# Kernel tuning notes

Hardware: AMD Instinct MI355X
Metric: run time of the kernel (lower is better)

The kernel has to match this reference:

```python
import jax, jax.numpy as jnp
import numpy as np
from jax import lax

CONF_T = 0.5
IOU_T = 0.5
STRIDE = 8.0
NA = 3            # anchors per cell
NO = 16           # x,y,w,h,obj,10 landmarks,cls
G = 80            # grid size for 640/8
K = 300           # max detections kept into NMS
ANCHORS = np.array([[4., 5.], [8., 10.], [13., 16.]], dtype=np.float32)


def _conv(x, w, b, stride):
    y = lax.conv_general_dilated(x, w, (stride, stride), 'SAME',
                                 dimension_numbers=('NCHW', 'OIHW', 'NCHW'))
    return jax.nn.silu(y + b[None, :, None, None])


def _nms_single(boxes, scores):
    # boxes [N,4] xyxy, scores [N] (0 where below conf threshold)
    top_scores, idx = lax.top_k(scores, K)
    b = boxes[idx]                                   # [K,4]
    x1, y1, x2, y2 = b[:, 0], b[:, 1], b[:, 2], b[:, 3]
    area = jnp.maximum(x2 - x1, 0.) * jnp.maximum(y2 - y1, 0.)
    ix1 = jnp.maximum(x1[:, None], x1[None, :])
    iy1 = jnp.maximum(y1[:, None], y1[None, :])
    ix2 = jnp.minimum(x2[:, None], x2[None, :])
    iy2 = jnp.minimum(y2[:, None], y2[None, :])
    inter = jnp.maximum(ix2 - ix1, 0.) * jnp.maximum(iy2 - iy1, 0.)
    iou = inter / (area[:, None] + area[None, :] - inter + 1e-7)   # [K,K]

    ar = jnp.arange(K)

    def body(i, keep):
        sup = keep[i] & (iou[i] > IOU_T) & (ar > i)
        return keep & ~sup

    keep = lax.fori_loop(0, K, body, jnp.ones((K,), bool))
    keep = keep & (top_scores > 0.)
    return jnp.concatenate(
        [b, top_scores[:, None], keep.astype(b.dtype)[:, None]], axis=-1)  # [K,6]


def setup_inputs() -> dict:
    key = jax.random.key(0)
    ks = jax.random.split(key, 9)
    s = 0.1
    return {
        'x':  jax.random.uniform(ks[0], (16, 3, 640, 640), jnp.float32),
        'W1': jax.random.normal(ks[1], (16, 3, 3, 3), jnp.float32) * s,
        'b1': jnp.zeros((16,), jnp.float32),
        'W2': jax.random.normal(ks[2], (32, 16, 3, 3), jnp.float32) * s,
        'b2': jnp.zeros((32,), jnp.float32),
        'W3': jax.random.normal(ks[3], (64, 32, 3, 3), jnp.float32) * s,
        'b3': jnp.zeros((64,), jnp.float32),
        'Wh': jax.random.normal(ks[4], (NA * NO, 64, 1, 1), jnp.float32) * s,
        'bh': jnp.zeros((NA * NO,), jnp.float32),
    }


def reference(x, W1, b1, W2, b2, W3, b3, Wh, bh):
    B = x.shape[0]
    # backbone: stride-8 conv stem (YOLOv5n-like)
    f = _conv(x, W1, b1, 2)      # [B,16,320,320]
    f = _conv(f, W2, b2, 2)      # [B,32,160,160]
    f = _conv(f, W3, b3, 2)      # [B,64,80,80]
    h = lax.conv_general_dilated(f, Wh, (1, 1), 'SAME',
                                 dimension_numbers=('NCHW', 'OIHW', 'NCHW'))
    h = h + bh[None, :, None, None]                  # [B,NA*NO,G,G]
    p = h.reshape(B, NA, NO, G, G).transpose(0, 1, 3, 4, 2)  # [B,NA,G,G,NO]
    p = jax.nn.sigmoid(p)

    gy, gx = jnp.meshgrid(jnp.arange(G, dtype=jnp.float32),
                          jnp.arange(G, dtype=jnp.float32), indexing='ij')
    grid = jnp.stack([gx, gy], axis=-1)              # [G,G,2]
    anchors = jnp.asarray(ANCHORS)

    xy = (p[..., 0:2] * 2. - 0.5 + grid[None, None]) * STRIDE
    wh = (p[..., 2:4] * 2.) ** 2 * anchors[None, :, None, None, :]
    score = p[..., 4] * p[..., 15]                   # obj * cls

    boxes = jnp.concatenate([xy - wh / 2., xy + wh / 2.], axis=-1)
    boxes = boxes.reshape(B, -1, 4)                  # [B,N,4]
    score = score.reshape(B, -1)                     # [B,N]
    score = jnp.where(score > CONF_T, score, 0.)

    return jax.vmap(_nms_single)(boxes, score)       # [B,K,6]
```

## Files before the change

### kernel.cpp

```cpp
#include <hip/hip_runtime.h>
#include <math.h>

#define BATCH 16
#define GRID  80
#define NANCH 3
#define KTOP  300
#define NBOX  (NANCH*GRID*GRID)
#define SORT_CAP 8192

__device__ __forceinline__ float sigmoidf_(float x){ return 1.0f/(1.0f+expf(-x)); }

template<int CIN,int COUT,int C,int ICCH,int HIN,int HOUT,int TX,int TY>
__global__ __launch_bounds__(256, 1) void conv3x3s2_v7(
    const float* __restrict__ in, const float* __restrict__ w,
    const float* __restrict__ bias, float* __restrict__ out)
{
  constexpr int NTX = TX/4, NTY = TY/2, NSP = NTX*NTY, OCG = COUT/C;
  static_assert(NSP*OCG == 256, "bad thread layout");
  static_assert(C==4 || C==8, "C must be 4 or 8");
  constexpr int HR = 2*TY+1, HC = 2*TX+1;
  constexpr int NB4  = HC/4;
  constexpr int PADC = ((HC+3)/4)*4 + 4;
  constexpr int ILDSC = HR*PADC;
  constexpr int TBX = HOUT/TX, TBY = HOUT/TY;
  static_assert(TBX*TX == HOUT && TBY*TY == HOUT, "no masking");
  constexpr int NCH  = CIN/ICCH;
  constexpr int NH4  = ICCH*HR*NB4;
  constexpr int NH1  = ICCH*HR;
  constexpr int NWT  = ICCH*9*COUT;
  constexpr int NLD4 = (NH4+255)/256;
  constexpr int NLD1 = (NH1+255)/256;
  constexpr int NLDW = (NWT+255)/256;
  __shared__ float ilds[2][ICCH*ILDSC];
  __shared__ float wlds[2][NWT];

  const int t  = threadIdx.x;
  const int sx = t % NTX;
  const int sy = (t / NTX) % NTY;
  const int og = t / NSP;
  int blk = blockIdx.x;
  const int bx = blk % TBX; blk /= TBX;
  const int by = blk % TBY; blk /= TBY;
  const int b  = blk;

  const int ix0 = bx*2*TX, iy0 = by*2*TY;
  const int ylim = (iy0 + HR <= HIN) ? HR : (HIN - iy0);
  const bool tail_ok = (ix0 + NB4*4 < HIN);

  float4 hreg[NLD4];
  float  treg[NLD1];
  float  wreg[NLDW];

  auto load_regs = [&](int c0){
    #pragma unroll
    for (int l=0;l<NLD4;++l){
      int i = t + 256*l;
      float4 v = make_float4(0.f,0.f,0.f,0.f);
      if (i < NH4){
        int c = i/(HR*NB4), rm = i - c*(HR*NB4);
        int r = rm/NB4, m = rm - r*NB4;
        if (r < ylim)
          v = *(const float4*)(in + (size_t)(b*CIN + c0 + c)*HIN*HIN
                                  + (size_t)(iy0+r)*HIN + ix0 + 4*m);
      }
      hreg[l] = v;
    }
    #pragma unroll
    for (int l=0;l<NLD1;++l){
      int i = t + 256*l;
      float v = 0.f;
      if (i < NH1){
        int c = i/HR, r = i - c*HR;
        if (r < ylim && tail_ok)
          v = in[(size_t)(b*CIN + c0 + c)*HIN*HIN + (size_t)(iy0+r)*HIN + ix0 + NB4*4];
      }
      treg[l] = v;
    }
    #pragma unroll
    for (int l=0;l<NLDW;++l){
      int i = t + 256*l;
      float v = 0.f;
      if (i < NWT){
        int oc  = i % COUT;
        int k   = (i / COUT) % 9;
        int icl = i / (9*COUT);
        v = w[((size_t)oc*CIN + c0+icl)*9 + k];
      }
      wreg[l] = v;
    }
  };

  auto write_lds = [&](int bufi){
    #pragma unroll
    for (int l=0;l<NLD4;++l){
      int i = t + 256*l;
      if (i < NH4){
        int c = i/(HR*NB4), rm = i - c*(HR*NB4);
        int r = rm/NB4, m = rm - r*NB4;
        *(float4*)(&ilds[bufi][c*ILDSC + r*PADC + 4*((r>>2)&1) + 4*m]) = hreg[l];
      }
    }
    #pragma unroll
    for (int l=0;l<NLD1;++l){
      int i = t + 256*l;
      if (i < NH1){
        int c = i/HR, r = i - c*HR;
        ilds[bufi][c*ILDSC + r*PADC + 4*((r>>2)&1) + NB4*4] = treg[l];
      }
    }
    #pragma unroll
    for (int l=0;l<NLDW;++l){
      int i = t + 256*l;
      if (i < NWT) wlds[bufi][i] = wreg[l];
    }
  };

  float acc[C][2][4];
  #pragma unroll
  for (int j=0;j<C;++j){
    float bv = bias[og*C+j];
    #pragma unroll
    for (int py=0;py<2;++py)
      #pragma unroll
      for (int px=0;px<4;++px) acc[j][py][px]=bv;
  }

  load_regs(0);
  write_lds(0);
  __syncthreads();

  #pragma unroll 1
  for (int ch=0; ch<NCH; ++ch){
    const int cur = ch & 1;
    if (ch+1 < NCH) load_regs((ch+1)*ICCH);

    #pragma unroll 1
    for (int icl=0; icl<ICCH; ++icl){
      const float* wpb = &wlds[cur][icl*9*COUT] + og*C;
      float4 wk0[9], wk1[9];
      #pragma unroll
      for (int k=0;k<9;++k){
        wk0[k] = *(const float4*)(wpb + k*COUT);
        if constexpr (C==8) wk1[k] = *(const float4*)(wpb + k*COUT + 4);
      }
      const float* ipb = &ilds[cur][icl*ILDSC] + 8*sx;
      float rw[5][12];
      #pragma unroll
      for (int r=0;r<5;++r){
        const int rr = 4*sy + r;
        const float* rp = ipb + rr*PADC + 4*((rr>>2)&1);
        #pragma unroll
        for (int m=0;m<3;++m){
          float4 v4 = *(const float4*)(rp + 4*m);
          rw[r][4*m+0]=v4.x; rw[r][4*m+1]=v4.y; rw[r][4*m+2]=v4.z; rw[r][4*m+3]=v4.w;
        }
      }
      #pragma unroll
      for (int py=0;py<2;++py)
        #pragma unroll
        for (int ky=0;ky<3;++ky)
          #pragma unroll
          for (int kx=0;kx<3;++kx){
            const float4 wa = wk0[ky*3+kx];
            #pragma unroll
            for (int px=0;px<4;++px){
              const float xv = rw[2*py+ky][2*px+kx];
              acc[0][py][px] += xv*wa.x; acc[1][py][px] += xv*wa.y;
              acc[2][py][px] += xv*wa.z; acc[3][py][px] += xv*wa.w;
            }
            if constexpr (C==8){
              const float4 wb = wk1[ky*3+kx];
              #pragma unroll
              for (int px=0;px<4;++px){
                const float xv = rw[2*py+ky][2*px+kx];
                acc[4][py][px] += xv*wb.x; acc[5][py][px] += xv*wb.y;
                acc[6][py][px] += xv*wb.z; acc[7][py][px] += xv*wb.w;
              }
            }
          }
    }

    if (ch+1 < NCH) write_lds((ch+1)&1);
    __syncthreads();
  }

  const int oxb = bx*TX + sx*4;
  #pragma unroll
  for (int j=0;j<C;++j){
    int oc = og*C+j;
    #pragma unroll
    for (int py=0;py<2;++py){
      int oy = by*TY + sy*2 + py;
      float4 o4;
      float z0=acc[j][py][0], z1=acc[j][py][1], z2=acc[j][py][2], z3=acc[j][py][3];
      o4.x = z0/(1.0f+expf(-z0));
      o4.y = z1/(1.0f+expf(-z1));
      o4.z = z2/(1.0f+expf(-z2));
      o4.w = z3/(1.0f+expf(-z3));
      *(float4*)(out + ((size_t)(b*COUT+oc)*HOUT + oy)*HOUT + oxb) = o4;
    }
  }
}

__global__ __launch_bounds__(256) void decode_kernel(
    const float* __restrict__ f3, const float* __restrict__ Wh,
    const float* __restrict__ bh, float* __restrict__ boxes,
    float* __restrict__ scores)
{
  int idx = blockIdx.x*256 + threadIdx.x;
  const int total = BATCH*NANCH*GRID*GRID;
  if (idx >= total) return;
  int gx = idx % GRID;
  int gy = (idx/GRID)%GRID;
  int a  = (idx/(GRID*GRID))%NANCH;
  int b  = idx/(GRID*GRID*NANCH);
  const float aw[3] = {4.0f, 8.0f, 13.0f};
  const float ah[3] = {5.0f, 10.0f, 16.0f};
  const int   chs[6] = {0,1,2,3,4,15};
  const float* f = f3 + (size_t)b*64*GRID*GRID + (size_t)gy*GRID + gx;
  float acc[6];
  #pragma unroll
  for (int j=0;j<6;j++) acc[j] = bh[a*16 + chs[j]];
  for (int ic=0; ic<64; ++ic){
    float v = f[(size_t)ic*GRID*GRID];
    #pragma unroll
    for (int j=0;j<6;j++) acc[j] += v * Wh[(size_t)(a*16+chs[j])*64 + ic];
  }
  float p0 = sigmoidf_(acc[0]);
  float p1 = sigmoidf_(acc[1]);
  float p2 = sigmoidf_(acc[2]);
  float p3 = sigmoidf_(acc[3]);
  float p4 = sigmoidf_(acc[4]);
  float p15= sigmoidf_(acc[5]);
  float cx = (p0*2.0f - 0.5f + (float)gx)*8.0f;
  float cy = (p1*2.0f - 0.5f + (float)gy)*8.0f;
  float ww = p2*2.0f; ww = ww*ww*aw[a];
  float hh = p3*2.0f; hh = hh*hh*ah[a];
  float sc = p4*p15;
  sc = (sc > 0.5f) ? sc : 0.0f;
  int bi = a*GRID*GRID + gy*GRID + gx;
  float* bo = boxes + ((size_t)b*NBOX + bi)*4;
  bo[0] = cx - ww*0.5f;
  bo[1] = cy - hh*0.5f;
  bo[2] = cx + ww*0.5f;
  bo[3] = cy + hh*0.5f;
  scores[(size_t)b*NBOX + bi] = sc;
}

__global__ __launch_bounds__(1024) void topk_kernel(
    const float* __restrict__ boxes, const float* __restrict__ scores,
    float* __restrict__ nmsbuf, int* __restrict__ mcnt)
{
  __shared__ unsigned long long keys[SORT_CAP];
  __shared__ int   cntM;
  __shared__ int   sel[KTOP];
  __shared__ float selsc[KTOP];
  __shared__ int   wsum[16];
  __shared__ float rs[16];
  __shared__ int   ri[16];
  __shared__ unsigned clm[(NBOX+31)/32];

  const int b = blockIdx.x;
  const int t = threadIdx.x;
  const int lane = t & 63, wv = t >> 6;
  const float* scp = scores + (size_t)b*NBOX;

  if (t == 0) cntM = 0;
  __syncthreads();

  for (int i=t; i<NBOX; i+=1024){
    float v = scp[i];
    if (v > 0.0f){
      int p = atomicAdd(&cntM, 1);
      if (p < SORT_CAP)
        keys[p] = ((unsigned long long)__float_as_uint(v) << 32)
                | (unsigned)(0xFFFFFFFFu - (unsigned)i);
    }
  }
  __syncthreads();
  const int M = cntM;
  if (t == 0) mcnt[b] = M;

  if (M <= SORT_CAP){
    int P = 64; while (P < M) P <<= 1;
    for (int i=t; i<P; i+=1024) if (i >= M) keys[i] = 0ULL;
    __syncthreads();
    for (int k=2; k<=P; k<<=1){
      for (int j=k>>1; j>0; j>>=1){
        for (int i=t; i<P; i+=1024){
          int ixj = i ^ j;
          if (ixj > i){
            unsigned long long a = keys[i], c = keys[ixj];
            bool up = ((i & k) == 0);
            if (up ? (a < c) : (a > c)){ keys[i] = c; keys[ixj] = a; }
          }
        }
        __syncthreads();
      }
    }
    const int top = (M < KTOP) ? M : KTOP;
    if (t < top){
      unsigned long long kk = keys[t];
      selsc[t] = __uint_as_float((unsigned)(kk >> 32));
      sel[t]   = (int)(0xFFFFFFFFu - (unsigned)(kk & 0xFFFFFFFFu));
    }
    if (M < KTOP){
      const int need = KTOP - M;
      const int C = (NBOX + 1023)/1024;
      int lo = t*C, hi = lo+C; if (hi > NBOX) hi = NBOX; if (lo > NBOX) lo = NBOX;
      int zc = 0;
      for (int i=lo;i<hi;i++) if (scp[i] <= 0.0f) zc++;
      int v = zc;
      #pragma unroll
      for (int off=1; off<64; off<<=1){
        int n = __shfl_up(v, off);
        if (lane >= off) v += n;
      }
      if (lane == 63) wsum[wv] = v;
      __syncthreads();
      if (t == 0){
        int a = 0;
        for (int w=0; w<16; w++){ int tmp = wsum[w]; wsum[w] = a; a += tmp; }
      }
      __syncthreads();
      int r = wsum[wv] + v - zc;
      for (int i=lo;i<hi;i++){
        if (scp[i] <= 0.0f){
          if (r < need){ sel[M+r] = i; selsc[M+r] = 0.0f; }
          r++;
        }
      }
    }
    __syncthreads();
  } else {
    for (int i=t; i<(NBOX+31)/32; i+=1024) clm[i] = 0u;
    __syncthreads();
    for (int k=0;k<KTOP;k++){
      float best = -2.0f; int bi = NBOX;
      for (int i=t;i<NBOX;i+=1024){
        if (!((clm[i>>5] >> (i&31)) & 1u)){
          float v = scp[i];
          if (v > best){ best=v; bi=i; }
        }
      }
      #pragma unroll
      for (int off=32; off>0; off>>=1){
        float ov = __shfl_down(best, off);
        int   oi = __shfl_down(bi,   off);
        if (ov > best || (ov == best && oi < bi)){ best=ov; bi=oi; }
      }
      if (lane == 0){ rs[wv]=best; ri[wv]=bi; }
      __syncthreads();
      if (t == 0){
        for (int w=1; w<16; w++)
          if (rs[w] > best || (rs[w] == best && ri[w] < bi)){ best=rs[w]; bi=ri[w]; }
        sel[k]=bi; selsc[k]=best; clm[bi>>5] |= (1u << (bi&31));
      }
      __syncthreads();
    }
  }

  if (t < KTOP){
    const float* bp = boxes + ((size_t)b*NBOX + sel[t])*4;
    float x1=bp[0], y1=bp[1], x2=bp[2], y2=bp[3];
    float* o = nmsbuf + ((size_t)b*KTOP + t)*6;
    o[0]=x1; o[1]=y1; o[2]=x2; o[3]=y2;
    o[4]=selsc[t];
    o[5]=fmaxf(x2-x1,0.0f)*fmaxf(y2-y1,0.0f);
  }
}

__global__ __launch_bounds__(64, 1) void nms_kernel(
    const float* __restrict__ nmsbuf, const int* __restrict__ mcnt,
    float* __restrict__ out)
{
  const int b = blockIdx.x;
  const int lane = threadIdx.x;
  int Mtop = mcnt[b]; if (Mtop > KTOP) Mtop = KTOP;
  float X1[5],Y1[5],X2[5],Y2[5],AR[5],SC[5];
  unsigned keepm = 0;
  #pragma unroll
  for (int s5=0; s5<5; ++s5){
    int j = lane + 64*s5;
    if (j < KTOP){
      const float* p = nmsbuf + ((size_t)b*KTOP + j)*6;
      X1[s5]=p[0]; Y1[s5]=p[1]; X2[s5]=p[2]; Y2[s5]=p[3];
      SC[s5]=p[4]; AR[s5]=p[5];
      keepm |= (1u << s5);
    } else { X1[s5]=0;Y1[s5]=0;X2[s5]=0;Y2[s5]=0;AR[s5]=0;SC[s5]=0; }
  }
  for (int i=0;i<Mtop;i++){
    const int iw = i & 63, is = i >> 6;
    unsigned km = __shfl(keepm, iw);
    if ((km >> is) & 1u){
      float sx1 = (is==0)?X1[0]:(is==1)?X1[1]:(is==2)?X1[2]:(is==3)?X1[3]:X1[4];
      float sy1 = (is==0)?Y1[0]:(is==1)?Y1[1]:(is==2)?Y1[2]:(is==3)?Y1[3]:Y1[4];
      float sx2 = (is==0)?X2[0]:(is==1)?X2[1]:(is==2)?X2[2]:(is==3)?X2[3]:X2[4];
      float sy2 = (is==0)?Y2[0]:(is==1)?Y2[1]:(is==2)?Y2[2]:(is==3)?Y2[3]:Y2[4];
      float sa  = (is==0)?AR[0]:(is==1)?AR[1]:(is==2)?AR[2]:(is==3)?AR[3]:AR[4];
      float bx1=__shfl(sx1,iw), by1=__shfl(sy1,iw);
      float bx2=__shfl(sx2,iw), by2=__shfl(sy2,iw);
      float ba =__shfl(sa ,iw);
      #pragma unroll
      for (int s5=0; s5<5; ++s5){
        int j = lane + 64*s5;
        if (((keepm >> s5) & 1u) && j > i){
          float ix1=fmaxf(bx1,X1[s5]);
          float iy1=fmaxf(by1,Y1[s5]);
          float ix2=fminf(bx2,X2[s5]);
          float iy2=fminf(by2,Y2[s5]);
          float inter=fmaxf(ix2-ix1,0.0f)*fmaxf(iy2-iy1,0.0f);
          float iou = inter/(ba+AR[s5]-inter+1e-7f);
          if (iou > 0.5f) keepm &= ~(1u << s5);
        }
      }
    }
  }
  #pragma unroll
  for (int s5=0; s5<5; ++s5){
    int j = lane + 64*s5;
    if (j < KTOP){
      float scv = SC[s5];
      float kf  = (((keepm >> s5) & 1u) && scv > 0.0f) ? 1.0f : 0.0f;
      float* o = out + ((size_t)b*KTOP + j)*6;
      o[0]=X1[s5]; o[1]=Y1[s5]; o[2]=X2[s5]; o[3]=Y2[s5];
      o[4]=scv; o[5]=kf;
    }
  }
}

extern "C" void kernel_launch(void* const* d_in, const int* in_sizes, int n_in,
                              void* d_out, int out_size, void* d_ws, size_t ws_size,
                              hipStream_t stream) {
  const float* x  = (const float*)d_in[0];
  const float* W1 = (const float*)d_in[1];
  const float* b1 = (const float*)d_in[2];
  const float* W2 = (const float*)d_in[3];
  const float* b2 = (const float*)d_in[4];
  const float* W3 = (const float*)d_in[5];
  const float* b3 = (const float*)d_in[6];
  const float* Wh = (const float*)d_in[7];
  const float* bh = (const float*)d_in[8];
  float* out = (float*)d_out;
  float* ws  = (float*)d_ws;

  float* f1     = ws;
  float* f2     = ws + 26214400;
  float* f3     = ws;
  float* boxes  = ws + 26214400;
  float* scores = boxes + 1228800;
  float* nmsbuf = scores + 307200;
  int*   mcnt   = (int*)(nmsbuf + 28800);

  conv3x3s2_v7<3,16,8,1,640,320,64,16><<<5*20*BATCH, 256, 0, stream>>>(x,  W1, b1, f1);
  conv3x3s2_v7<16,32,8,2,320,160,32,16><<<5*10*BATCH, 256, 0, stream>>>(f1, W2, b2, f2);
  conv3x3s2_v7<32,64,4,4,160,80,16,8><<<5*10*BATCH, 256, 0, stream>>>(f2, W3, b3, f3);

  decode_kernel<<<(BATCH*NANCH*GRID*GRID+255)/256, 256, 0, stream>>>(f3, Wh, bh, boxes, scores);
  topk_kernel<<<BATCH, 1024, 0, stream>>>(boxes, scores, nmsbuf, mcnt);
  nms_kernel<<<BATCH, 64, 0, stream>>>(nmsbuf, mcnt, out);
}
```

Before: 403.7 us.

## Fuse third conv with head decode and raise occupancy hint for conv2

Adds a kernel that computes the third 3x3 stride-2 conv and, inside the same block, stages the activated tile in shared memory to run the 1x1 head and box decode for the six needed channels. This removes the f3 write/read round trip and one kernel launch. Separately, conv2's launch bounds now request 4 waves per EU instead of 1, trading register budget for occupancy. The fused kernel reuses shared memory between the conv and decode phases, which adds an extra barrier and some per-block head-weight loads.

Measured after the change: 386.9 us. -4.2%, faster.

```diff
diff --git a/kernel.cpp b/kernel.cpp
--- a/kernel.cpp
+++ b/kernel.cpp
@@ -10,8 +10,8 @@
 
 __device__ __forceinline__ float sigmoidf_(float x){ return 1.0f/(1.0f+expf(-x)); }
 
-template<int CIN,int COUT,int C,int ICCH,int HIN,int HOUT,int TX,int TY>
-__global__ __launch_bounds__(256, 1) void conv3x3s2_v7(
+template<int CIN,int COUT,int C,int ICCH,int HIN,int HOUT,int TX,int TY,int MINW>
+__global__ __launch_bounds__(256, MINW) void conv3x3s2_v7(
     const float* __restrict__ in, const float* __restrict__ w,
     const float* __restrict__ bias, float* __restrict__ out)
 {
@@ -202,49 +202,235 @@
   }
 }
 
-__global__ __launch_bounds__(256) void decode_kernel(
-    const float* __restrict__ f3, const float* __restrict__ Wh,
-    const float* __restrict__ bh, float* __restrict__ boxes,
-    float* __restrict__ scores)
+__global__ __launch_bounds__(256, 1) void conv3_decode_fused(
+    const float* __restrict__ in,
+    const float* __restrict__ w,
+    const float* __restrict__ bias,
+    const float* __restrict__ wh,
+    const float* __restrict__ bh,
+    float* __restrict__ boxes, float* __restrict__ scores)
 {
-  int idx = blockIdx.x*256 + threadIdx.x;
-  const int total = BATCH*NANCH*GRID*GRID;
-  if (idx >= total) return;
-  int gx = idx % GRID;
-  int gy = (idx/GRID)%GRID;
-  int a  = (idx/(GRID*GRID))%NANCH;
-  int b  = idx/(GRID*GRID*NANCH);
-  const float aw[3] = {4.0f, 8.0f, 13.0f};
-  const float ah[3] = {5.0f, 10.0f, 16.0f};
-  const int   chs[6] = {0,1,2,3,4,15};
-  const float* f = f3 + (size_t)b*64*GRID*GRID + (size_t)gy*GRID + gx;
-  float acc[6];
+  constexpr int CIN=32, COUT=64, C=4, ICCH=4, HIN=160, TX=16, TY=8;
+  constexpr int NTX=TX/4, NTY=TY/2, NSP=NTX*NTY;
+  constexpr int HR=2*TY+1, HC=2*TX+1;
+  constexpr int NB4=HC/4;
+  constexpr int PADC=((HC+3)/4)*4+4;
+  constexpr int ILDSC=HR*PADC;
+  constexpr int TBX=5, TBY=10;
+  constexpr int NCH=CIN/ICCH;
+  constexpr int NH4=ICCH*HR*NB4;
+  constexpr int NH1=ICCH*HR;
+  constexpr int NWT=ICCH*9*COUT;
+  constexpr int NLD4=(NH4+255)/256, NLD1=(NH1+255)/256, NLDW=(NWT+255)/256;
+  __shared__ float smem[11232];
+  float* ildsb = smem;
+  float* wldsb = smem + 5440;
+  float* f3l   = smem;
+  float* whl   = smem + 10048;
+  float* bhl   = smem + 11200;
+
+  const int t  = threadIdx.x;
+  const int sx = t % NTX;
+  const int sy = (t / NTX) % NTY;
+  const int og = t / NSP;
+  int blk = blockIdx.x;
+  const int bx = blk % TBX; blk /= TBX;
+  const int by = blk % TBY; blk /= TBY;
+  const int b  = blk;
+
+  {
+    const int chs[6] = {0,1,2,3,4,15};
+    for (int i=t; i<1152; i+=256){
+      int row = i >> 6, ic = i & 63;
+      int a = row/6, j = row - 6*a;
+      whl[i] = wh[(size_t)(a*16+chs[j])*64 + ic];
+    }
+    if (t < 18){ int a=t/6, j=t-6*a; bhl[t] = bh[a*16+chs[j]]; }
+  }
+
+  const int ix0 = bx*2*TX, iy0 = by*2*TY;
+  const int ylim = (iy0 + HR <= HIN) ? HR : (HIN - iy0);
+  const bool tail_ok = (ix0 + NB4*4 < HIN);
+
+  float4 hreg[NLD4];
+  float  treg[NLD1];
+  float  wreg[NLDW];
+
+  auto load_regs = [&](int c0){
+    #pragma unroll
+    for (int l=0;l<NLD4;++l){
+      int i = t + 256*l;
+      float4 v = make_float4(0.f,0.f,0.f,0.f);
+      if (i < NH4){
+        int c = i/(HR*NB4), rm = i - c*(HR*NB4);
+        int r = rm/NB4, m = rm - r*NB4;
+        if (r < ylim)
+          v = *(const float4*)(in + (size_t)(b*CIN + c0 + c)*HIN*HIN
+                                  + (size_t)(iy0+r)*HIN + ix0 + 4*m);
+      }
+      hreg[l] = v;
+    }
+    #pragma unroll
+    for (int l=0;l<NLD1;++l){
+      int i = t + 256*l;
+      float v = 0.f;
+      if (i < NH1){
+        int c = i/HR, r = i - c*HR;
+        if (r < ylim && tail_ok)
+          v = in[(size_t)(b*CIN + c0 + c)*HIN*HIN + (size_t)(iy0+r)*HIN + ix0 + NB4*4];
+      }
+      treg[l] = v;
+    }
+    #pragma unroll
+    for (int l=0;l<NLDW;++l){
+      int i = t + 256*l;
+      float v = 0.f;
+      if (i < NWT){
+        int oc  = i % COUT;
+        int k   = (i / COUT) % 9;
+        int icl = i / (9*COUT);
+        v = w[((size_t)oc*CIN + c0+icl)*9 + k];
+      }
+      wreg[l] = v;
+    }
+  };
+
+  auto write_lds = [&](int bufi){
+    #pragma unroll
+    for (int l=0;l<NLD4;++l){
+      int i = t + 256*l;
+      if (i < NH4){
+        int c = i/(HR*NB4), rm = i - c*(HR*NB4);
+        int r = rm/NB4, m = rm - r*NB4;
+        *(float4*)(&ildsb[bufi*(ICCH*ILDSC) + c*ILDSC + r*PADC + 4*((r>>2)&1) + 4*m]) = hreg[l];
+      }
+    }
+    #pragma unroll
+    for (int l=0;l<NLD1;++l){
+      int i = t + 256*l;
+      if (i < NH1){
+        int c = i/HR, r = i - c*HR;
+        ildsb[bufi*(ICCH*ILDSC) + c*ILDSC + r*PADC + 4*((r>>2)&1) + NB4*4] = treg[l];
+      }
+    }
+    #pragma unroll
+    for (int l=0;l<NLDW;++l){
+      int i = t + 256*l;
+      if (i < NWT) wldsb[bufi*NWT + i] = wreg[l];
+    }
+  };
+
+  float acc[C][2][4];
   #pragma unroll
-  for (int j=0;j<6;j++) acc[j] = bh[a*16 + chs[j]];
-  for (int ic=0; ic<64; ++ic){
-    float v = f[(size_t)ic*GRID*GRID];
-    #pragma unroll
-    for (int j=0;j<6;j++) acc[j] += v * Wh[(size_t)(a*16+chs[j])*64 + ic];
-  }
-  float p0 = sigmoidf_(acc[0]);
-  float p1 = sigmoidf_(acc[1]);
-  float p2 = sigmoidf_(acc[2]);
-  float p3 = sigmoidf_(acc[3]);
-  float p4 = sigmoidf_(acc[4]);
-  float p15= sigmoidf_(acc[5]);
-  float cx = (p0*2.0f - 0.5f + (float)gx)*8.0f;
-  float cy = (p1*2.0f - 0.5f + (float)gy)*8.0f;
-  float ww = p2*2.0f; ww = ww*ww*aw[a];
-  float hh = p3*2.0f; hh = hh*hh*ah[a];
-  float sc = p4*p15;
-  sc = (sc > 0.5f) ? sc : 0.0f;
-  int bi = a*GRID*GRID + gy*GRID + gx;
-  float* bo = boxes + ((size_t)b*NBOX + bi)*4;
-  bo[0] = cx - ww*0.5f;
-  bo[1] = cy - hh*0.5f;
-  bo[2] = cx + ww*0.5f;
-  bo[3] = cy + hh*0.5f;
-  scores[(size_t)b*NBOX + bi] = sc;
+  for (int j=0;j<C;++j){
+    float bv = bias[og*C+j];
+    #pragma unroll
+    for (int py=0;py<2;++py)
+      #pragma unroll
+      for (int px=0;px<4;++px) acc[j][py][px]=bv;
+  }
+
+  load_regs(0);
+  write_lds(0);
+  __syncthreads();
+
+  #pragma unroll 1
+  for (int ch=0; ch<NCH; ++ch){
+    const int cur = ch & 1;
+    if (ch+1 < NCH) load_regs((ch+1)*ICCH);
+
+    #pragma unroll 1
+    for (int icl=0; icl<ICCH; ++icl){
+      const float* wpb = &wldsb[cur*NWT + icl*9*COUT] + og*C;
+      float4 wk0[9];
+      #pragma unroll
+      for (int k=0;k<9;++k) wk0[k] = *(const float4*)(wpb + k*COUT);
+      const float* ipb = &ildsb[cur*(ICCH*ILDSC) + icl*ILDSC] + 8*sx;
+      float rw[5][12];
+      #pragma unroll
+      for (int r=0;r<5;++r){
+        const int rr = 4*sy + r;
+        const float* rp = ipb + rr*PADC + 4*((rr>>2)&1);
+        #pragma unroll
+        for (int m=0;m<3;++m){
+          float4 v4 = *(const float4*)(rp + 4*m);
+          rw[r][4*m+0]=v4.x; rw[r][4*m+1]=v4.y; rw[r][4*m+2]=v4.z; rw[r][4*m+3]=v4.w;
+        }
+      }
+      #pragma unroll
+      for (int py=0;py<2;++py)
+        #pragma unroll
+        for (int ky=0;ky<3;++ky)
+          #pragma unroll
+          for (int kx=0;kx<3;++kx){
+            const float4 wa = wk0[ky*3+kx];
+            #pragma unroll
+            for (int px=0;px<4;++px){
+              const float xv = rw[2*py+ky][2*px+kx];
+              acc[0][py][px] += xv*wa.x; acc[1][py][px] += xv*wa.y;
+              acc[2][py][px] += xv*wa.z; acc[3][py][px] += xv*wa.w;
+            }
+          }
+    }
+
+    if (ch+1 < NCH) write_lds((ch+1)&1);
+    __syncthreads();
+  }
+
+  #pragma unroll
+  for (int j=0;j<C;++j){
+    int oc = og*C+j;
+    #pragma unroll
+    for (int py=0;py<2;++py)
+      #pragma unroll
+      for (int px=0;px<4;++px){
+        int pxidx = (sy*2+py)*16 + sx*4+px;
+        float z = acc[j][py][px];
+        f3l[pxidx*68 + oc] = z/(1.0f+expf(-z));
+      }
+  }
+  __syncthreads();
+
+  const float awv[3] = {4.0f, 8.0f, 13.0f};
+  const float ahv[3] = {5.0f, 10.0f, 16.0f};
+  for (int q=t; q<384; q+=256){
+    int a = q >> 7, p = q & 127;
+    float ac[6];
+    #pragma unroll
+    for (int j=0;j<6;++j) ac[j] = bhl[a*6+j];
+    const float* fp = f3l + p*68;
+    const float* wp = whl + a*6*64;
+    #pragma unroll 4
+    for (int ic=0; ic<64; ic+=4){
+      float4 fv = *(const float4*)(fp + ic);
+      #pragma unroll
+      for (int j=0;j<6;++j){
+        float4 wv = *(const float4*)(wp + j*64 + ic);
+        ac[j] += fv.x*wv.x; ac[j] += fv.y*wv.y;
+        ac[j] += fv.z*wv.z; ac[j] += fv.w*wv.w;
+      }
+    }
+    float p0 = sigmoidf_(ac[0]);
+    float p1 = sigmoidf_(ac[1]);
+    float p2 = sigmoidf_(ac[2]);
+    float p3 = sigmoidf_(ac[3]);
+    float p4 = sigmoidf_(ac[4]);
+    float p15= sigmoidf_(ac[5]);
+    int gx = bx*16 + (p & 15), gy = by*8 + (p >> 4);
+    float cx = (p0*2.0f - 0.5f + (float)gx)*8.0f;
+    float cy = (p1*2.0f - 0.5f + (float)gy)*8.0f;
+    float ww = p2*2.0f; ww = ww*ww*awv[a];
+    float hh = p3*2.0f; hh = hh*hh*ahv[a];
+    float sc = p4*p15;
+    sc = (sc > 0.5f) ? sc : 0.0f;
+    int bi = a*GRID*GRID + gy*GRID + gx;
+    float* bo = boxes + ((size_t)b*NBOX + bi)*4;
+    bo[0] = cx - ww*0.5f;
+    bo[1] = cy - hh*0.5f;
+    bo[2] = cx + ww*0.5f;
+    bo[3] = cy + hh*0.5f;
+    scores[(size_t)b*NBOX + bi] = sc;
+  }
 }
 
 __global__ __launch_bounds__(1024) void topk_kernel(
@@ -306,8 +492,8 @@
     }
     if (M < KTOP){
       const int need = KTOP - M;
-      const int C = (NBOX + 1023)/1024;
-      int lo = t*C, hi = lo+C; if (hi > NBOX) hi = NBOX; if (lo > NBOX) lo = NBOX;
+      const int Cc = (NBOX + 1023)/1024;
+      int lo = t*Cc, hi = lo+Cc; if (hi > NBOX) hi = NBOX; if (lo > NBOX) lo = NBOX;
       int zc = 0;
       for (int i=lo;i<hi;i++) if (scp[i] <= 0.0f) zc++;
       int v = zc;
@@ -446,17 +632,15 @@
 
   float* f1     = ws;
   float* f2     = ws + 26214400;
-  float* f3     = ws;
-  float* boxes  = ws + 26214400;
+  float* boxes  = ws;
   float* scores = boxes + 1228800;
   float* nmsbuf = scores + 307200;
   int*   mcnt   = (int*)(nmsbuf + 28800);
 
-  conv3x3s2_v7<3,16,8,1,640,320,64,16><<<5*20*BATCH, 256, 0, stream>>>(x,  W1, b1, f1);
-  conv3x3s2_v7<16,32,8,2,320,160,32,16><<<5*10*BATCH, 256, 0, stream>>>(f1, W2, b2, f2);
-  conv3x3s2_v7<32,64,4,4,160,80,16,8><<<5*10*BATCH, 256, 0, stream>>>(f2, W3, b3, f3);
-
-  decode_kernel<<<(BATCH*NANCH*GRID*GRID+255)/256, 256, 0, stream>>>(f3, Wh, bh, boxes, scores);
+  conv3x3s2_v7<3,16,8,1,640,320,64,16,1><<<5*20*BATCH, 256, 0, stream>>>(x,  W1, b1, f1);
+  conv3x3s2_v7<16,32,8,2,320,160,32,16,4><<<5*10*BATCH, 256, 0, stream>>>(f1, W2, b2, f2);
+  conv3_decode_fused<<<5*10*BATCH, 256, 0, stream>>>(f2, W3, b3, Wh, bh, boxes, scores);
+
   topk_kernel<<<BATCH, 1024, 0, stream>>>(boxes, scores, nmsbuf, mcnt);
   nms_kernel<<<BATCH, 64, 0, stream>>>(nmsbuf, mcnt, out);
 }
```
